# Performance work log

Hardware: AMD Instinct MI355X
Metric: run time of the kernel (lower is better)

The kernel has to match this reference:

```python
import jax, jax.numpy as jnp
import numpy as np

I, H, L, D, O = 256, 512, 2, 2, 8  # input, hidden, layers, directions, output


def _lstm_dir(x, h0, c0, w_ih, w_hh, b, reverse):
    """One LSTM direction. x: [S,B,in] -> hidden seq [S,B,H] (time-aligned)."""
    def step(carry, xt):
        h, c = carry
        gates = xt @ w_ih.T + h @ w_hh.T + b            # [B,4H], PyTorch gate order i,f,g,o
        i, f, g, o = jnp.split(gates, 4, axis=-1)
        c = jax.nn.sigmoid(f) * c + jax.nn.sigmoid(i) * jnp.tanh(g)
        h = jax.nn.sigmoid(o) * jnp.tanh(c)
        return (h, c), h
    _, ys = jax.lax.scan(step, (h0, c0), x, reverse=reverse)
    return ys


def setup_inputs() -> dict:
    key = jax.random.key(0)
    ks = jax.random.split(key, 32)
    s = 1.0 / np.sqrt(H)
    inp = {
        "input_seq": jax.random.normal(ks[0], (64, 512, I), jnp.float32),
        "h0": jax.random.normal(ks[1], (L * D, 64, H), jnp.float32),
        "c0": jax.random.normal(ks[2], (L * D, 64, H), jnp.float32),
    }
    k = 3
    for l in range(L):
        in_dim = I if l == 0 else H * D
        for d, tag in enumerate("fb"):
            inp[f"w_ih_{l}{tag}"] = jax.random.uniform(ks[k], (4 * H, in_dim), jnp.float32, -s, s); k += 1
            inp[f"w_hh_{l}{tag}"] = jax.random.uniform(ks[k], (4 * H, H), jnp.float32, -s, s); k += 1
            inp[f"b_{l}{tag}"] = jax.random.uniform(ks[k], (4 * H,), jnp.float32, -s, s); k += 1  # b_ih + b_hh combined
    inp["fc_w"] = jax.random.uniform(ks[k], (O, H * D), jnp.float32, -s, s); k += 1
    inp["fc_b"] = jax.random.uniform(ks[k], (O,), jnp.float32, -s, s)
    return inp


def reference(input_seq, h0, c0,
              w_ih_0f, w_hh_0f, b_0f, w_ih_0b, w_hh_0b, b_0b,
              w_ih_1f, w_hh_1f, b_1f, w_ih_1b, w_hh_1b, b_1b,
              fc_w, fc_b):
    x = jnp.transpose(input_seq, (1, 0, 2))  # [S,B,I] time-major
    params = [
        ((w_ih_0f, w_hh_0f, b_0f), (w_ih_0b, w_hh_0b, b_0b)),
        ((w_ih_1f, w_hh_1f, b_1f), (w_ih_1b, w_hh_1b, b_1b)),
    ]
    for l, (pf, pb) in enumerate(params):
        fwd = _lstm_dir(x, h0[2 * l], c0[2 * l], *pf, reverse=False)
        bwd = _lstm_dir(x, h0[2 * l + 1], c0[2 * l + 1], *pb, reverse=True)
        x = jnp.concatenate([fwd, bwd], axis=-1)  # [S,B,2H]
    last = x[-1]                                   # [B,2H] == output[:, -1, :]
    pred = last @ fc_w.T + fc_b                    # fc then slice last step (same math)
    return pred[None]                              # torch.stack([pred], dim=0) -> [1,B,O]
```

## Files before the change

kernel.cpp:

```cpp
#include <hip/hip_runtime.h>
#include <hip/hip_bf16.h>


typedef __attribute__((ext_vector_type(8))) __bf16 bf16x8;
typedef __attribute__((ext_vector_type(4))) float f32x4;

struct Params {
  const float *input_seq, *h0, *c0;
  const float *w_ih_0f, *w_hh_0f, *b_0f;
  const float *w_ih_0b, *w_hh_0b, *b_0b;
  const float *w_ih_1f, *w_hh_1f, *b_1f;
  const float *w_ih_1b, *w_hh_1b, *b_1b;
  const float *fc_w, *fc_b;
  float* out;
  unsigned* flags;
  unsigned* stepf;
  __bf16* xT;
  __bf16* Wp0f; __bf16* Wp0b;
  __bf16* Wp1f; __bf16* Wp1b;
  __bf16* y0;
  __bf16* y1f;
  __bf16* h1binit;
  __bf16* h1bout;
  float* bp;
};

__device__ __forceinline__ float sigm(float x) { return 1.f / (1.f + __expf(-x)); }
__device__ __forceinline__ float tanh_fast(float x) {
  return 1.f - 2.f / (1.f + __expf(2.f * x));
}

__device__ __forceinline__ void phase_barrier(unsigned* pf, int wg, int tid, unsigned phase) {
  __syncthreads();
  if (tid == 0) {
    __builtin_amdgcn_fence(__ATOMIC_RELEASE, "agent");
    __hip_atomic_store(pf + wg, phase, __ATOMIC_RELAXED, __HIP_MEMORY_SCOPE_AGENT);
  }
  bool ok;
  unsigned it = 0;
  do {
    unsigned v = __hip_atomic_load(pf + tid, __ATOMIC_RELAXED, __HIP_MEMORY_SCOPE_AGENT);
    ok = (v >= phase) || (++it > 200000u);
    if (!ok) __builtin_amdgcn_s_sleep(8);
  } while (!__syncthreads_and(ok));
  __builtin_amdgcn_fence(__ATOMIC_ACQUIRE, "agent");
}

__device__ __forceinline__ bool group_wait128(const unsigned* base, int lane,
                                              unsigned need, bool fast) {
  for (unsigned it = 0;; ++it) {
    unsigned v0 = __hip_atomic_load(base + (size_t)lane * 16, __ATOMIC_RELAXED,
                                    __HIP_MEMORY_SCOPE_AGENT);
    unsigned v1 = __hip_atomic_load(base + (size_t)(lane + 64) * 16, __ATOMIC_RELAXED,
                                    __HIP_MEMORY_SCOPE_AGENT);
    bool ok = (v0 >= need) && (v1 >= need);
    if (__ballot(ok) == ~0ull) break;
    if (it > 1000000u) return false;
    if (!fast) __builtin_amdgcn_s_sleep(1);
  }
  asm volatile("" ::: "memory");
  return true;
}

__device__ __forceinline__ void flag_store(unsigned* a, unsigned v, bool fast) {
  if (fast) __hip_atomic_store(a, v, __ATOMIC_RELAXED, __HIP_MEMORY_SCOPE_WORKGROUP);
  else      __hip_atomic_store(a, v, __ATOMIC_RELAXED, __HIP_MEMORY_SCOPE_AGENT);
}

__device__ __forceinline__ void pointwise_t(f32x4 g4, int lane, float& c,
                                            __bf16* rowptr, bool fast) {
  float cj = sigm(g4[1]) * c + sigm(g4[0]) * tanh_fast(g4[2]);
  c = cj;
  float h = sigm(g4[3]) * tanh_fast(cj);
  __bf16 hb = (__bf16)h;
  unsigned short hu; __builtin_memcpy(&hu, &hb, 2);
  unsigned v0 = (unsigned)hu | (__shfl_down((unsigned)hu, 16) << 16);
  unsigned long long pk = (unsigned long long)v0 |
                          ((unsigned long long)__shfl_down(v0, 32) << 32);
  if (lane < 16) {
    if (fast)
      __hip_atomic_store((unsigned long long*)rowptr, pk,
                         __ATOMIC_RELAXED, __HIP_MEMORY_SCOPE_WORKGROUP);
    else
      __hip_atomic_store((unsigned long long*)rowptr, pk,
                         __ATOMIC_RELAXED, __HIP_MEMORY_SCOPE_AGENT);
  }
}

__global__ __launch_bounds__(256, 1) void lstm_kernel(Params p) {
  const int tid  = threadIdx.x;
  const int wg   = blockIdx.x;
  const unsigned gtid = wg * 256 + tid;
  const int lane = tid & 63;
  const int wv   = tid >> 6;
  const int colq = lane & 15;
  const int quad = lane >> 4;

  {
    unsigned xcd = __builtin_amdgcn_s_getreg(20 | (31 << 11));
    if (tid == 0) p.flags[512 + wg] = xcd;
  }
  {
    int row = gtid >> 1, half = gtid & 1;
    int t = row >> 6, b = row & 63;
    const float* src = p.input_seq + ((size_t)b * 512 + t) * 256 + half * 128;
    __bf16* dst = p.xT + (size_t)row * 256 + half * 128;
    for (int i = 0; i < 128; i += 8) {
      bf16x8 v;
      #pragma unroll
      for (int j = 0; j < 8; ++j) v[j] = (__bf16)src[i + j];
      *(bf16x8*)(dst + i) = v;
    }
  }
  for (unsigned task = gtid; task < 2u * 2048 * 6; task += 65536) {
    unsigned dir = task / (2048 * 6);
    unsigned rr = (task / 6) % 2048;
    unsigned ch = task % 6;
    unsigned R = (rr & 3) * 512 + (rr >> 2);
    const float* wih = dir ? p.w_ih_0b : p.w_ih_0f;
    const float* whh = dir ? p.w_hh_0b : p.w_hh_0f;
    __bf16* dst = (dir ? p.Wp0b : p.Wp0f) + (size_t)rr * 768;
    const float* src; unsigned kd;
    if (ch < 4) { src = whh + (size_t)R * 512 + ch * 128;        kd = ch * 128; }
    else        { src = wih + (size_t)R * 256 + (ch - 4) * 128;  kd = 512 + (ch - 4) * 128; }
    for (int i = 0; i < 128; i += 8) {
      bf16x8 v;
      #pragma unroll
      for (int j = 0; j < 8; ++j) v[j] = (__bf16)src[i + j];
      *(bf16x8*)(dst + kd + i) = v;
    }
  }
  for (unsigned task = gtid; task < 2u * 2048 * 12; task += 65536) {
    unsigned dir = task / (2048 * 12);
    unsigned rr = (task / 12) % 2048;
    unsigned ch = task % 12;
    unsigned R = (rr & 3) * 512 + (rr >> 2);
    const float* wih = dir ? p.w_ih_1b : p.w_ih_1f;
    const float* whh = dir ? p.w_hh_1b : p.w_hh_1f;
    __bf16* dst = (dir ? p.Wp1b : p.Wp1f) + (size_t)rr * 1536;
    const float* src; unsigned kd;
    if (ch < 4) { src = whh + (size_t)R * 512 + ch * 128;         kd = ch * 128; }
    else        { src = wih + (size_t)R * 1024 + (ch - 4) * 128;  kd = 512 + (ch - 4) * 128; }
    for (int i = 0; i < 128; i += 8) {
      bf16x8 v;
      #pragma unroll
      for (int j = 0; j < 8; ++j) v[j] = (__bf16)src[i + j];
      *(bf16x8*)(dst + kd + i) = v;
    }
  }
  if (gtid < 4u * 2048) {
    unsigned arr = gtid >> 11, rr = gtid & 2047;
    unsigned R = (rr & 3) * 512 + (rr >> 2);
    const float* src = arr == 0 ? p.b_0f : arr == 1 ? p.b_0b : arr == 2 ? p.b_1f : p.b_1b;
    p.bp[arr * 2048 + rr] = src[R];
  }
  if (gtid < 4u * 4096) {
    unsigned dl = gtid >> 12;
    unsigned e = (gtid & 4095) * 8;
    unsigned b = e >> 9, u = e & 511;
    const float* src = p.h0 + (size_t)dl * 64 * 512 + (size_t)b * 512 + u;
    __bf16* dst;
    if (dl == 0)      dst = p.y0 + ((size_t)0 * 64 + b) * 1024 + u;
    else if (dl == 1) dst = p.y0 + ((size_t)513 * 64 + b) * 1024 + 512 + u;
    else if (dl == 2) dst = p.y1f + ((size_t)0 * 64 + b) * 512 + u;
    else              dst = p.h1binit + (size_t)b * 512 + u;
    bf16x8 v;
    #pragma unroll
    for (int j = 0; j < 8; ++j) v[j] = (__bf16)src[j];
    *(bf16x8*)dst = v;
  }

  phase_barrier(p.flags, wg, tid, 1u);

  bool fast;
  {
    const unsigned* xt = p.flags + 512;
    const int r = wg & 7;
    unsigned x0 = xt[r];
    bool ok = true;
    for (int k = 1; k < 32; ++k) ok &= (xt[r + 8 * k] == x0);
    unsigned mask = 0;
    for (int rr = 0; rr < 8; ++rr) mask |= 1u << (xt[rr] & 31);
    ok &= (__popc(mask) == 8);
    fast = ok;
  }

  {
    const int g = wg & 7;
    const bool fwd = g < 4;
    const int bg = g & 3;
    const int ug = wg >> 3;
    const int bbase = bg * 16;
    const int uglob = ug * 16 + wv * 4;
    const int colbase = uglob * 4;
    const __bf16* Wp = fwd ? p.Wp0f : p.Wp0b;
    bf16x8 wfH[16], wfI[8];
    #pragma unroll
    for (int kb = 0; kb < 16; ++kb)
      wfH[kb] = *(const bf16x8*)(Wp + (size_t)(colbase + colq) * 768 + kb * 32 + quad * 8);
    #pragma unroll
    for (int kb = 0; kb < 8; ++kb)
      wfI[kb] = *(const bf16x8*)(Wp + (size_t)(colbase + colq) * 768 + 512 + kb * 32 + quad * 8);
    const f32x4 bias4 = *(const f32x4*)(p.bp + (fwd ? 0 : 1) * 2048 + colbase + quad * 4);
    float c = p.c0[(size_t)(fwd ? 0 : 1) * 64 * 512 +
                   (size_t)(bbase + colq) * 512 + uglob + quad];
    const int dcol = fwd ? 0 : 512;
    unsigned* gfl = p.stepf + (size_t)g * 128 * 16;
    bool alive = true;
    for (int s = 0; s < 512; ++s) {
      const int t = fwd ? s : 511 - s;
      const int slabA = fwd ? t : t + 2;
      const __bf16* aX = p.xT + ((size_t)t * 64 + bbase + colq) * 256 + quad * 8;
      bf16x8 xf[8];
      #pragma unroll
      for (int kb = 0; kb < 8; ++kb) xf[kb] = *(const bf16x8*)(aX + kb * 32);
      if (s > 0 && alive) alive = group_wait128(gfl, lane, (unsigned)s, fast);
      const __bf16* aH = p.y0 + ((size_t)slabA * 64 + bbase + colq) * 1024 + dcol + quad * 8;
      f32x4 accX = bias4;
      f32x4 accH0 = {0.f, 0.f, 0.f, 0.f}, accH1 = {0.f, 0.f, 0.f, 0.f};
      #pragma unroll
      for (int kb = 0; kb < 8; ++kb)
        accX = __builtin_amdgcn_mfma_f32_16x16x32_bf16(wfI[kb], xf[kb], accX, 0, 0, 0);
      #pragma unroll
      for (int kb = 0; kb < 8; ++kb)
        accH0 = __builtin_amdgcn_mfma_f32_16x16x32_bf16(wfH[kb], *(const bf16x8*)(aH + kb * 32), accH0, 0, 0, 0);
      #pragma unroll
      for (int kb = 0; kb < 8; ++kb)
        accH1 = __builtin_amdgcn_mfma_f32_16x16x32_bf16(wfH[8 + kb], *(const bf16x8*)(aH + (8 + kb) * 32), accH1, 0, 0, 0);
      f32x4 g4 = accX + accH0 + accH1;
      pointwise_t(g4, lane, c,
        p.y0 + ((size_t)(t + 1) * 64 + bbase + colq) * 1024 + dcol + uglob, fast);
      if (s < 511) {
        asm volatile("s_waitcnt vmcnt(0)" ::: "memory");
        if (lane == 0)
          flag_store(gfl + (size_t)(ug * 4 + wv) * 16, (unsigned)(s + 1), fast);
      }
    }
  }
  phase_barrier(p.flags, wg, tid, 2u);

  if ((wg & 7) < 4) {
    const int bg = wg & 7;
    const int ug = wg >> 3;
    const int bbase = bg * 16;
    const int uglob = ug * 16 + wv * 4;
    const int colbase = uglob * 4;
    bf16x8 wfH[16], wfX[32];
    #pragma unroll
    for (int kb = 0; kb < 16; ++kb)
      wfH[kb] = *(const bf16x8*)(p.Wp1f + (size_t)(colbase + colq) * 1536 + kb * 32 + quad * 8);
    #pragma unroll
    for (int kb = 0; kb < 32; ++kb)
      wfX[kb] = *(const bf16x8*)(p.Wp1f + (size_t)(colbase + colq) * 1536 + 512 + kb * 32 + quad * 8);
    const f32x4 bias4 = *(const f32x4*)(p.bp + 2 * 2048 + colbase + quad * 4);
    float c = p.c0[(size_t)2 * 64 * 512 +
                   (size_t)(bbase + colq) * 512 + uglob + quad];
    unsigned* gfl = p.stepf + (size_t)(8 + bg) * 128 * 16;
    bool alive = true;
    for (int t = 0; t < 512; ++t) {
      const __bf16* aX = p.y0 + ((size_t)(t + 1) * 64 + bbase + colq) * 1024 + quad * 8;
      bf16x8 xf[32];
      #pragma unroll
      for (int kb = 0; kb < 32; ++kb) xf[kb] = *(const bf16x8*)(aX + kb * 32);
      if (t > 0 && alive) alive = group_wait128(gfl, lane, (unsigned)t, fast);
      const __bf16* aH = p.y1f + ((size_t)t * 64 + bbase + colq) * 512 + quad * 8;
      f32x4 accH = bias4;
      f32x4 accX0 = {0.f, 0.f, 0.f, 0.f}, accX1 = {0.f, 0.f, 0.f, 0.f};
      #pragma unroll
      for (int kb = 0; kb < 16; ++kb)
        accH = __builtin_amdgcn_mfma_f32_16x16x32_bf16(wfH[kb], *(const bf16x8*)(aH + kb * 32), accH, 0, 0, 0);
      #pragma unroll
      for (int kb = 0; kb < 16; ++kb)
        accX0 = __builtin_amdgcn_mfma_f32_16x16x32_bf16(wfX[kb], xf[kb], accX0, 0, 0, 0);
      #pragma unroll
      for (int kb = 0; kb < 16; ++kb)
        accX1 = __builtin_amdgcn_mfma_f32_16x16x32_bf16(wfX[16 + kb], xf[16 + kb], accX1, 0, 0, 0);
      f32x4 g4 = accH + accX0 + accX1;
      pointwise_t(g4, lane, c,
        p.y1f + ((size_t)(t + 1) * 64 + bbase + colq) * 512 + uglob, fast);
      if (t < 511) {
        asm volatile("s_waitcnt vmcnt(0)" ::: "memory");
        if (lane == 0)
          flag_store(gfl + (size_t)(ug * 4 + wv) * 16, (unsigned)(t + 1), fast);
      }
    }
  } else {
    const int bg = (wg & 7) - 4;
    const int ug = wg >> 3;
    const int bbase = bg * 16;
    const int uglob = ug * 16 + wv * 4;
    const int colbase = uglob * 4;
    const __bf16* aH = p.h1binit + (size_t)(bbase + colq) * 512 + quad * 8;
    const __bf16* aX = p.y0 + ((size_t)512 * 64 + bbase + colq) * 1024 + quad * 8;
    const __bf16* wrow = p.Wp1b + (size_t)(colbase + colq) * 1536;
    const f32x4 bias4 = *(const f32x4*)(p.bp + 3 * 2048 + colbase + quad * 4);
    f32x4 accH = bias4;
    f32x4 accX0 = {0.f, 0.f, 0.f, 0.f}, accX1 = {0.f, 0.f, 0.f, 0.f};
    #pragma unroll
    for (int kb = 0; kb < 16; ++kb)
      accH = __builtin_amdgcn_mfma_f32_16x16x32_bf16(*(const bf16x8*)(wrow + kb * 32 + quad * 8),
                                                     *(const bf16x8*)(aH + kb * 32), accH, 0, 0, 0);
    #pragma unroll
    for (int kb = 0; kb < 16; ++kb)
      accX0 = __builtin_amdgcn_mfma_f32_16x16x32_bf16(*(const bf16x8*)(wrow + (16 + kb) * 32 + quad * 8),
                                                      *(const bf16x8*)(aX + kb * 32), accX0, 0, 0, 0);
    #pragma unroll
    for (int kb = 0; kb < 16; ++kb)
      accX1 = __builtin_amdgcn_mfma_f32_16x16x32_bf16(*(const bf16x8*)(wrow + (32 + kb) * 32 + quad * 8),
                                                      *(const bf16x8*)(aX + (16 + kb) * 32), accX1, 0, 0, 0);
    f32x4 g4 = accH + accX0 + accX1;
    float c = p.c0[(size_t)3 * 64 * 512 +
                   (size_t)(bbase + colq) * 512 + uglob + quad];
    pointwise_t(g4, lane, c,
      p.h1bout + (size_t)(bbase + colq) * 512 + uglob, true);
  }
  phase_barrier(p.flags, wg, tid, 3u);

  if (wg < 8) {
    const int b = wg * 8 + (tid >> 5);
    const int o = (tid >> 2) & 7;
    const int ks = tid & 3;
    const int k0 = ks * 256;
    const __bf16* l1 = p.y1f + ((size_t)512 * 64 + b) * 512;
    const __bf16* l2 = p.h1bout + (size_t)b * 512;
    const __bf16* hsrc = (ks < 2) ? (l1 + k0) : (l2 + k0 - 512);
    const float* w = p.fc_w + (size_t)o * 1024 + k0;
    float acc = 0.f;
    for (int k = 0; k < 256; ++k) acc += (float)hsrc[k] * w[k];
    acc += __shfl_down(acc, 2, 4);
    acc += __shfl_down(acc, 1, 4);
    if (ks == 0) p.out[b * 8 + o] = acc + p.fc_b[o];
  }
}

extern "C" void kernel_launch(void* const* d_in, const int* in_sizes, int n_in,
                              void* d_out, int out_size, void* d_ws, size_t ws_size,
                              hipStream_t stream) {
  char* ws = (char*)d_ws;
  Params p;
  p.input_seq = (const float*)d_in[0];
  p.h0 = (const float*)d_in[1];
  p.c0 = (const float*)d_in[2];
  p.w_ih_0f = (const float*)d_in[3];  p.w_hh_0f = (const float*)d_in[4];  p.b_0f = (const float*)d_in[5];
  p.w_ih_0b = (const float*)d_in[6];  p.w_hh_0b = (const float*)d_in[7];  p.b_0b = (const float*)d_in[8];
  p.w_ih_1f = (const float*)d_in[9];  p.w_hh_1f = (const float*)d_in[10]; p.b_1f = (const float*)d_in[11];
  p.w_ih_1b = (const float*)d_in[12]; p.w_hh_1b = (const float*)d_in[13]; p.b_1b = (const float*)d_in[14];
  p.fc_w = (const float*)d_in[15];    p.fc_b = (const float*)d_in[16];
  p.out = (float*)d_out;

  const size_t STEPF_BYTES = (size_t)12 * 128 * 64;
  const size_t SYNC_BYTES = 4096 + STEPF_BYTES;
  size_t off = 0;
  p.flags  = (unsigned*)(ws + off); off += 4096;
  p.stepf  = (unsigned*)(ws + off); off += STEPF_BYTES;
  p.xT     = (__bf16*)(ws + off);   off += (size_t)512 * 64 * 256 * 2;
  p.Wp0f   = (__bf16*)(ws + off);   off += (size_t)2048 * 768 * 2;
  p.Wp0b   = (__bf16*)(ws + off);   off += (size_t)2048 * 768 * 2;
  p.Wp1f   = (__bf16*)(ws + off);   off += (size_t)2048 * 1536 * 2;
  p.Wp1b   = (__bf16*)(ws + off);   off += (size_t)2048 * 1536 * 2;
  p.y0     = (__bf16*)(ws + off);   off += (size_t)514 * 64 * 1024 * 2;
  p.y1f    = (__bf16*)(ws + off);   off += (size_t)513 * 64 * 512 * 2;
  p.h1binit= (__bf16*)(ws + off);   off += (size_t)64 * 512 * 2;
  p.h1bout = (__bf16*)(ws + off);   off += (size_t)64 * 512 * 2;
  p.bp     = (float*)(ws + off);    off += (size_t)4 * 2048 * 4;
  (void)ws_size; (void)in_sizes; (void)n_in; (void)out_size;

  hipMemsetAsync(d_ws, 0, SYNC_BYTES, stream);
  lstm_kernel<<<dim3(256), dim3(256), 0, stream>>>(p);
}
```

Before: 6.258 ms.

## Stage layer-1 input weights in LDS, stream x loads, store h per-lane

Half of the layer-1 forward input-projection weights move from registers into shared memory and are reloaded from LDS each step. This lowers register pressure, since the previous version held 48 bf16x8 weight fragments plus 32 x fragments. The x loads are now issued one by one and consumed by the MFMA chain instead of being held in a preloaded array, and the input projection is computed before the flag wait so it can overlap the wait. The pointwise step drops the cross-lane shuffle packing and has each lane atomically store its own 2-byte h value, which costs more, smaller stores.

```diff
diff --git a/kernel.cpp b/kernel.cpp
--- a/kernel.cpp
+++ b/kernel.cpp
@@ -67,24 +67,19 @@
   else      __hip_atomic_store(a, v, __ATOMIC_RELAXED, __HIP_MEMORY_SCOPE_AGENT);
 }
 
-__device__ __forceinline__ void pointwise_t(f32x4 g4, int lane, float& c,
-                                            __bf16* rowptr, bool fast) {
+__device__ __forceinline__ void pointwise_t2(f32x4 g4, float& c,
+                                             __bf16* eptr, bool fast) {
   float cj = sigm(g4[1]) * c + sigm(g4[0]) * tanh_fast(g4[2]);
   c = cj;
   float h = sigm(g4[3]) * tanh_fast(cj);
   __bf16 hb = (__bf16)h;
   unsigned short hu; __builtin_memcpy(&hu, &hb, 2);
-  unsigned v0 = (unsigned)hu | (__shfl_down((unsigned)hu, 16) << 16);
-  unsigned long long pk = (unsigned long long)v0 |
-                          ((unsigned long long)__shfl_down(v0, 32) << 32);
-  if (lane < 16) {
-    if (fast)
-      __hip_atomic_store((unsigned long long*)rowptr, pk,
-                         __ATOMIC_RELAXED, __HIP_MEMORY_SCOPE_WORKGROUP);
-    else
-      __hip_atomic_store((unsigned long long*)rowptr, pk,
-                         __ATOMIC_RELAXED, __HIP_MEMORY_SCOPE_AGENT);
-  }
+  if (fast)
+    __hip_atomic_store((unsigned short*)eptr, hu,
+                       __ATOMIC_RELAXED, __HIP_MEMORY_SCOPE_WORKGROUP);
+  else
+    __hip_atomic_store((unsigned short*)eptr, hu,
+                       __ATOMIC_RELAXED, __HIP_MEMORY_SCOPE_AGENT);
 }
 
 __global__ __launch_bounds__(256, 1) void lstm_kernel(Params p) {
@@ -95,6 +90,8 @@
   const int wv   = tid >> 6;
   const int colq = lane & 15;
   const int quad = lane >> 4;
+
+  __shared__ __bf16 wlds[32768];
 
   {
     unsigned xcd = __builtin_amdgcn_s_getreg(20 | (31 << 11));
@@ -211,16 +208,15 @@
       const int t = fwd ? s : 511 - s;
       const int slabA = fwd ? t : t + 2;
       const __bf16* aX = p.xT + ((size_t)t * 64 + bbase + colq) * 256 + quad * 8;
-      bf16x8 xf[8];
-      #pragma unroll
-      for (int kb = 0; kb < 8; ++kb) xf[kb] = *(const bf16x8*)(aX + kb * 32);
+      f32x4 accX = bias4;
+      #pragma unroll
+      for (int kb = 0; kb < 8; ++kb) {
+        bf16x8 xv = *(const bf16x8*)(aX + kb * 32);
+        accX = __builtin_amdgcn_mfma_f32_16x16x32_bf16(wfI[kb], xv, accX, 0, 0, 0);
+      }
       if (s > 0 && alive) alive = group_wait128(gfl, lane, (unsigned)s, fast);
       const __bf16* aH = p.y0 + ((size_t)slabA * 64 + bbase + colq) * 1024 + dcol + quad * 8;
-      f32x4 accX = bias4;
       f32x4 accH0 = {0.f, 0.f, 0.f, 0.f}, accH1 = {0.f, 0.f, 0.f, 0.f};
-      #pragma unroll
-      for (int kb = 0; kb < 8; ++kb)
-        accX = __builtin_amdgcn_mfma_f32_16x16x32_bf16(wfI[kb], xf[kb], accX, 0, 0, 0);
       #pragma unroll
       for (int kb = 0; kb < 8; ++kb)
         accH0 = __builtin_amdgcn_mfma_f32_16x16x32_bf16(wfH[kb], *(const bf16x8*)(aH + kb * 32), accH0, 0, 0, 0);
@@ -228,8 +224,8 @@
       for (int kb = 0; kb < 8; ++kb)
         accH1 = __builtin_amdgcn_mfma_f32_16x16x32_bf16(wfH[8 + kb], *(const bf16x8*)(aH + (8 + kb) * 32), accH1, 0, 0, 0);
       f32x4 g4 = accX + accH0 + accH1;
-      pointwise_t(g4, lane, c,
-        p.y0 + ((size_t)(t + 1) * 64 + bbase + colq) * 1024 + dcol + uglob, fast);
+      pointwise_t2(g4, c,
+        p.y0 + ((size_t)(t + 1) * 64 + bbase + colq) * 1024 + dcol + uglob + quad, fast);
       if (s < 511) {
         asm volatile("s_waitcnt vmcnt(0)" ::: "memory");
         if (lane == 0)
@@ -245,13 +241,21 @@
     const int bbase = bg * 16;
     const int uglob = ug * 16 + wv * 4;
     const int colbase = uglob * 4;
-    bf16x8 wfH[16], wfX[32];
+    bf16x8 wfH[16], wfX2[16];
     #pragma unroll
     for (int kb = 0; kb < 16; ++kb)
       wfH[kb] = *(const bf16x8*)(p.Wp1f + (size_t)(colbase + colq) * 1536 + kb * 32 + quad * 8);
-    #pragma unroll
-    for (int kb = 0; kb < 32; ++kb)
-      wfX[kb] = *(const bf16x8*)(p.Wp1f + (size_t)(colbase + colq) * 1536 + 512 + kb * 32 + quad * 8);
+    {
+      const __bf16* wsrc = p.Wp1f + (size_t)(colbase + colq) * 1536 + 512;
+      #pragma unroll
+      for (int kb = 0; kb < 16; ++kb) {
+        bf16x8 w = *(const bf16x8*)(wsrc + kb * 32 + quad * 8);
+        *(bf16x8*)(wlds + ((size_t)(wv * 16 + kb) * 64 + lane) * 8) = w;
+      }
+      #pragma unroll
+      for (int kb = 0; kb < 16; ++kb)
+        wfX2[kb] = *(const bf16x8*)(wsrc + (16 + kb) * 32 + quad * 8);
+    }
     const f32x4 bias4 = *(const f32x4*)(p.bp + 2 * 2048 + colbase + quad * 4);
     float c = p.c0[(size_t)2 * 64 * 512 +
                    (size_t)(bbase + colq) * 512 + uglob + quad];
@@ -259,25 +263,30 @@
     bool alive = true;
     for (int t = 0; t < 512; ++t) {
       const __bf16* aX = p.y0 + ((size_t)(t + 1) * 64 + bbase + colq) * 1024 + quad * 8;
-      bf16x8 xf[32];
-      #pragma unroll
-      for (int kb = 0; kb < 32; ++kb) xf[kb] = *(const bf16x8*)(aX + kb * 32);
+      f32x4 accX0 = bias4, accX1 = {0.f, 0.f, 0.f, 0.f};
+      #pragma unroll
+      for (int kb = 0; kb < 16; ++kb) {
+        bf16x8 xv = *(const bf16x8*)(aX + kb * 32);
+        bf16x8 wx = *(const bf16x8*)(wlds + ((size_t)(wv * 16 + kb) * 64 + lane) * 8);
+        accX0 = __builtin_amdgcn_mfma_f32_16x16x32_bf16(wx, xv, accX0, 0, 0, 0);
+      }
+      #pragma unroll
+      for (int kb = 0; kb < 16; ++kb) {
+        bf16x8 xv = *(const bf16x8*)(aX + (16 + kb) * 32);
+        accX1 = __builtin_amdgcn_mfma_f32_16x16x32_bf16(wfX2[kb], xv, accX1, 0, 0, 0);
+      }
       if (t > 0 && alive) alive = group_wait128(gfl, lane, (unsigned)t, fast);
       const __bf16* aH = p.y1f + ((size_t)t * 64 + bbase + colq) * 512 + quad * 8;
-      f32x4 accH = bias4;
-      f32x4 accX0 = {0.f, 0.f, 0.f, 0.f}, accX1 = {0.f, 0.f, 0.f, 0.f};
-      #pragma unroll
-      for (int kb = 0; kb < 16; ++kb)
-        accH = __builtin_amdgcn_mfma_f32_16x16x32_bf16(wfH[kb], *(const bf16x8*)(aH + kb * 32), accH, 0, 0, 0);
-      #pragma unroll
-      for (int kb = 0; kb < 16; ++kb)
-        accX0 = __builtin_amdgcn_mfma_f32_16x16x32_bf16(wfX[kb], xf[kb], accX0, 0, 0, 0);
-      #pragma unroll
-      for (int kb = 0; kb < 16; ++kb)
-        accX1 = __builtin_amdgcn_mfma_f32_16x16x32_bf16(wfX[16 + kb], xf[16 + kb], accX1, 0, 0, 0);
-      f32x4 g4 = accH + accX0 + accX1;
-      pointwise_t(g4, lane, c,
-        p.y1f + ((size_t)(t + 1) * 64 + bbase + colq) * 512 + uglob, fast);
+      f32x4 accH0 = {0.f, 0.f, 0.f, 0.f}, accH1 = {0.f, 0.f, 0.f, 0.f};
+      #pragma unroll
+      for (int kb = 0; kb < 8; ++kb)
+        accH0 = __builtin_amdgcn_mfma_f32_16x16x32_bf16(wfH[kb], *(const bf16x8*)(aH + kb * 32), accH0, 0, 0, 0);
+      #pragma unroll
+      for (int kb = 0; kb < 8; ++kb)
+        accH1 = __builtin_amdgcn_mfma_f32_16x16x32_bf16(wfH[8 + kb], *(const bf16x8*)(aH + (8 + kb) * 32), accH1, 0, 0, 0);
+      f32x4 g4 = accX0 + accX1 + accH0 + accH1;
+      pointwise_t2(g4, c,
+        p.y1f + ((size_t)(t + 1) * 64 + bbase + colq) * 512 + uglob + quad, fast);
       if (t < 511) {
         asm volatile("s_waitcnt vmcnt(0)" ::: "memory");
         if (lane == 0)
@@ -311,8 +320,8 @@
     f32x4 g4 = accH + accX0 + accX1;
     float c = p.c0[(size_t)3 * 64 * 512 +
                    (size_t)(bbase + colq) * 512 + uglob + quad];
-    pointwise_t(g4, lane, c,
-      p.h1bout + (size_t)(bbase + colq) * 512 + uglob, true);
+    pointwise_t2(g4, c,
+      p.h1bout + (size_t)(bbase + colq) * 512 + uglob + quad, true);
   }
   phase_barrier(p.flags, wg, tid, 3u);
 
```

Result: faster. 5.839 ms (-6.7%).
